# Kernel optimization log

Hardware: AMD Instinct MI355X
Metric: run time of the kernel (lower is better)

## Reference

```python
import jax, jax.numpy as jnp
import numpy as np

B, L, D, H, S = 4, 4096, 1024, 16, 4
DH = D // H


def setup_inputs() -> dict:
    key = jax.random.key(0)
    ks = jax.random.split(key, 12)
    std = 0.02
    inp = {
        "x": jax.random.normal(ks[0], (B, L, D), jnp.float32),
        "scale_logits": jax.random.normal(ks[1], (S,), jnp.float32),
        "wq": jax.random.normal(ks[2], (D, D), jnp.float32) * std,
        "bq": jnp.zeros((D,), jnp.float32),
        "wk": jax.random.normal(ks[3], (D, D), jnp.float32) * std,
        "bk": jnp.zeros((D,), jnp.float32),
        "wv": jax.random.normal(ks[4], (D, D), jnp.float32) * std,
        "bv": jnp.zeros((D,), jnp.float32),
        "wo": jax.random.normal(ks[5], (D, D), jnp.float32) * std,
        "bo": jnp.zeros((D,), jnp.float32),
        "ws": jax.random.normal(ks[6], (S, D, D), jnp.float32) * std,  # per-scale Linear weights (out,in)
        "bs": jax.random.normal(ks[7], (S, D), jnp.float32) * std,
    }
    return inp


def reference(x, scale_logits, wq, bq, wk, bk, wv, bv, wo, bo, ws, bs):
    # q/k/v projections; kept flat (B,L,D) since the torch code re-flattens before scale proj
    qf = x @ wq.T + bq
    kf = x @ wk.T + bk
    vf = x @ wv.T + bv
    # per-scale linear projection, vectorized over scales: (B,S,L,D)
    sq = jnp.einsum('bld,sed->bsle', qf, ws) + bs[None, :, None, :]
    sk = jnp.einsum('bld,sed->bsle', kf, ws) + bs[None, :, None, :]
    sv = jnp.einsum('bld,sed->bsle', vf, ws) + bs[None, :, None, :]
    sq = sq.reshape(B, S, L, H, DH)
    sk = sk.reshape(B, S, L, H, DH)
    sv = sv.reshape(B, S, L, H, DH)
    # faithful to torch: matmul over last two dims of (B,L,H,dh) -> per-position
    # head-mixing scores of shape (B,S,L,H,H)
    scale = 1.0 / np.sqrt(DH).astype(np.float32)
    scores = jnp.einsum('bslhd,bslgd->bslhg', sq, sk) * scale
    attn = jax.nn.softmax(scores, axis=-1)
    out = jnp.einsum('bslhg,bslgd->bslhd', attn, sv)  # (B,S,L,H,DH)
    w = jax.nn.softmax(scale_logits, axis=0)  # (S,)
    combined = jnp.einsum('s,bslhd->blhd', w, out).reshape(B, L, D)
    return combined @ wo.T + bo
```

## Files before the change

### kernel.cpp

```cpp
#include <hip/hip_runtime.h>


typedef unsigned short u16;
typedef __attribute__((ext_vector_type(8))) short s16x8;
typedef __attribute__((ext_vector_type(8))) unsigned short u16x8;
typedef __attribute__((ext_vector_type(4))) float f32x4;

#define MM 16384
#define DDIM 1024
#define DDSQ 1048576ull

__device__ __forceinline__ u16 f2bf(float f) {
  unsigned u = __float_as_uint(f);
  u = (u + 0x7FFFu + ((u >> 16) & 1u)) >> 16;
  return (u16)u;
}
__device__ __forceinline__ float b2f(u16 b) {
  return __uint_as_float(((unsigned)b) << 16);
}
__device__ __forceinline__ void gload_lds16(const void* g, void* l) {
  __builtin_amdgcn_global_load_lds(
      (const __attribute__((address_space(1))) void*)g,
      (__attribute__((address_space(3))) void*)l, 16, 0, 0);
}

__global__ __launch_bounds__(256) void k_f32_to_bf16(
    const float* __restrict__ in, u16* __restrict__ out, int n4) {
  int i = blockIdx.x * 256 + threadIdx.x;
  if (i >= n4) return;
  float4 v = reinterpret_cast<const float4*>(in)[i];
  ushort4 o;
  o.x = f2bf(v.x); o.y = f2bf(v.y); o.z = f2bf(v.z); o.w = f2bf(v.w);
  reinterpret_cast<ushort4*>(out)[i] = o;
}

__global__ __launch_bounds__(256) void k_transpose_bf16(
    const float* __restrict__ wq, const float* __restrict__ wk,
    const float* __restrict__ wv, u16* __restrict__ out) {
  __shared__ float tile[32][33];
  const float* src = (blockIdx.z == 0) ? wq : (blockIdx.z == 1) ? wk : wv;
  u16* dst = out + (size_t)blockIdx.z * DDSQ;
  int tx = threadIdx.x, ty = threadIdx.y;
  int bx = blockIdx.x * 32, by = blockIdx.y * 32;
#pragma unroll
  for (int i = 0; i < 4; ++i)
    tile[ty + 8 * i][tx] = src[(size_t)(by + ty + 8 * i) * DDIM + bx + tx];
  __syncthreads();
#pragma unroll
  for (int i = 0; i < 4; ++i)
    dst[(size_t)(bx + ty + 8 * i) * DDIM + by + tx] = f2bf(tile[tx][ty + 8 * i]);
}

__global__ __launch_bounds__(256) void k_bias_fuse(
    const float* __restrict__ ws, const float* __restrict__ bq,
    const float* __restrict__ bk, const float* __restrict__ bv,
    const float* __restrict__ bs, float* __restrict__ bf) {
  int idx = blockIdx.y;
  int s = idx / 3, t = idx - s * 3;
  const float* bt = (t == 0) ? bq : (t == 1) ? bk : bv;
  int lane = threadIdx.x & 63, wid = threadIdx.x >> 6;
  int e = blockIdx.x * 4 + wid;
  const float* wr = ws + (size_t)s * DDSQ + (size_t)e * DDIM;
  float p = 0.f;
  for (int j = lane; j < DDIM; j += 64) p += wr[j] * bt[j];
#pragma unroll
  for (int off = 32; off > 0; off >>= 1) p += __shfl_xor(p, off);
  if (lane == 0) bf[idx * DDIM + e] = p + bs[s * DDIM + e];
}

template <typename OutT>
__global__ __launch_bounds__(256) void k_gemm_bt(
    const u16* __restrict__ A, const u16* __restrict__ B, OutT* __restrict__ C,
    const float* __restrict__ bias, int M, int N, int K,
    size_t za, size_t zb, size_t zc, size_t zbias, int zmode) {
  __shared__ u16 lds_a[128 * 32];
  __shared__ u16 lds_b[128 * 32];

  int z = blockIdx.x >> 3;
  int n_blk = blockIdx.x & 7;
  int m_blk = blockIdx.y;
  if (zmode == 1) { A += (size_t)(z / 3) * za; B += (size_t)(z % 3) * zb; }
  else            { A += (size_t)z * za;       B += (size_t)z * zb; }
  C += (size_t)z * zc;
  const float* biasz = bias ? (bias + (size_t)z * zbias) : nullptr;

  int m0 = m_blk * 128, n0 = n_blk * 128;
  int tid = threadIdx.x;
  int lane = tid & 63, wid = tid >> 6;
  int wm = wid >> 1, wn = wid & 1;

  f32x4 acc[4][4] = {};

  auto stage = [&](int k0) {
#pragma unroll
    for (int i = 0; i < 2; ++i) {
      int c = wid * 2 + i;
      int row = c * 16 + (lane >> 2);
      int col = (lane & 3) * 8;
      gload_lds16(A + (size_t)(m0 + row) * K + k0 + col, &lds_a[c * 512]);
      gload_lds16(B + (size_t)(n0 + row) * K + k0 + col, &lds_b[c * 512]);
    }
  };

  stage(0);
  int ar = (wm * 64 + (lane & 15)) * 32 + (lane >> 4) * 8;
  int br = (wn * 64 + (lane & 15)) * 32 + (lane >> 4) * 8;
  for (int k0 = 0;;) {
    __syncthreads();
    s16x8 af[4], bfr[4];
#pragma unroll
    for (int mi = 0; mi < 4; ++mi)
      af[mi] = *reinterpret_cast<const s16x8*>(&lds_a[ar + mi * 16 * 32]);
#pragma unroll
    for (int ni = 0; ni < 4; ++ni)
      bfr[ni] = *reinterpret_cast<const s16x8*>(&lds_b[br + ni * 16 * 32]);
#pragma unroll
    for (int mi = 0; mi < 4; ++mi)
#pragma unroll
      for (int ni = 0; ni < 4; ++ni)
        acc[mi][ni] = __builtin_amdgcn_mfma_f32_16x16x32_bf16(
            af[mi], bfr[ni], acc[mi][ni], 0, 0, 0);
    k0 += 32;
    if (k0 >= K) break;
    __syncthreads();
    stage(k0);
  }

#pragma unroll
  for (int mi = 0; mi < 4; ++mi) {
#pragma unroll
    for (int ni = 0; ni < 4; ++ni) {
      int colg = n0 + wn * 64 + ni * 16 + (lane & 15);
      float badd = biasz ? biasz[colg] : 0.f;
#pragma unroll
      for (int r = 0; r < 4; ++r) {
        int rowg = m0 + wm * 64 + mi * 16 + ((lane >> 4) << 2) + r;
        float v = acc[mi][ni][r] + badd;
        if constexpr (sizeof(OutT) == 2) C[(size_t)rowg * N + colg] = f2bf(v);
        else                             C[(size_t)rowg * N + colg] = v;
      }
    }
  }
}

__global__ __launch_bounds__(512, 2) void k_gemm256(
    const u16* __restrict__ A, const u16* __restrict__ B, u16* __restrict__ C,
    const float* __restrict__ bias, int M, int N, int K,
    size_t za, size_t zb, size_t zc, size_t zbias, int nbx) {
  __shared__ u16 lds[3][2][8192];

  int z = blockIdx.x / nbx;
  int nb = blockIdx.x - z * nbx;
  const u16* Ag = A + (size_t)z * za;
  const u16* Bg = B + (size_t)z * zb;
  u16* Cg = C + (size_t)z * zc;
  const float* biasz = bias + (size_t)z * zbias;

  int m0 = blockIdx.y * 256, n0 = nb * 256;
  int tid = threadIdx.x;
  int lane = tid & 63, wid = tid >> 6;
  int wm = wid >> 2, wn = wid & 3;
  int NT = K >> 5;

  int scb = ((lane & 3) * 16) ^ (((lane >> 3) & 3) << 4);
  const char* srcA[2]; const char* srcB[2]; int ldsc[2];
#pragma unroll
  for (int r = 0; r < 2; ++r) {
    int c = r * 8 + wid;
    int row = c * 16 + (lane >> 2);
    srcA[r] = (const char*)Ag + ((size_t)(m0 + row) * K) * 2 + scb;
    srcB[r] = (const char*)Bg + ((size_t)(n0 + row) * K) * 2 + scb;
    ldsc[r] = c * 1024;
  }
  char* lbase = (char*)&lds[0][0][0];

  int fxor = ((lane >> 4) * 16) ^ (((lane >> 1) & 3) << 4);
  int aoff = (wm * 128 + (lane & 15)) * 64 + fxor;
  int boff = (wn * 64 + (lane & 15)) * 64 + fxor;

  f32x4 acc[8][4] = {};

#define STAGE_A(kt, rg)                                                   \
  {                                                                       \
    _Pragma("unroll") for (int r = 0; r < 2; ++r)                         \
        gload_lds16(srcA[r] + (size_t)(kt) * 64,                          \
                    lbase + (rg) * 32768 + ldsc[r]);                      \
  }
#define STAGE_B(kt, rg)                                                   \
  {                                                                       \
    _Pragma("unroll") for (int r = 0; r < 2; ++r)                         \
        gload_lds16(srcB[r] + (size_t)(kt) * 64,                          \
                    lbase + (rg) * 32768 + 16384 + ldsc[r]);              \
  }

  STAGE_A(0, 0); STAGE_B(0, 0);
  STAGE_A(1, 1); STAGE_B(1, 1);
  __builtin_amdgcn_sched_barrier(0);
  asm volatile("s_waitcnt vmcnt(4)" ::: "memory");
  __builtin_amdgcn_sched_barrier(0);
  __builtin_amdgcn_s_barrier();

  int ring = 0;
  for (int t = 0; t < NT; ++t) {
    int t2 = (t + 2 < NT) ? t + 2 : NT - 1;
    int rg2 = ring + 2; if (rg2 >= 3) rg2 -= 3;
    const char* bA = lbase + ring * 32768;
    const char* bB = bA + 16384;

    s16x8 fb[4], fa[4];
#pragma unroll
    for (int ni = 0; ni < 4; ++ni)
      fb[ni] = *(const s16x8*)(bB + boff + ni * 1024);
#pragma unroll
    for (int mi = 0; mi < 4; ++mi)
      fa[mi] = *(const s16x8*)(bA + aoff + mi * 1024);
    STAGE_A(t2, rg2);
    __builtin_amdgcn_sched_barrier(0);
    __builtin_amdgcn_s_barrier();
    asm volatile("s_waitcnt lgkmcnt(0)" ::: "memory");
    __builtin_amdgcn_sched_barrier(0);
    __builtin_amdgcn_s_setprio(1);
#pragma unroll
    for (int mi = 0; mi < 4; ++mi)
#pragma unroll
      for (int ni = 0; ni < 4; ++ni)
        acc[mi][ni] = __builtin_amdgcn_mfma_f32_16x16x32_bf16(
            fa[mi], fb[ni], acc[mi][ni], 0, 0, 0);
    __builtin_amdgcn_s_setprio(0);
    __builtin_amdgcn_sched_barrier(0);
    __builtin_amdgcn_s_barrier();

    s16x8 fa2[4];
#pragma unroll
    for (int mi = 0; mi < 4; ++mi)
      fa2[mi] = *(const s16x8*)(bA + aoff + 4096 + mi * 1024);
    STAGE_B(t2, rg2);
    __builtin_amdgcn_sched_barrier(0);
    asm volatile("s_waitcnt vmcnt(4)" ::: "memory");
    __builtin_amdgcn_sched_barrier(0);
    __builtin_amdgcn_s_barrier();
    asm volatile("s_waitcnt lgkmcnt(0)" ::: "memory");
    __builtin_amdgcn_sched_barrier(0);
    __builtin_amdgcn_s_setprio(1);
#pragma unroll
    for (int mi = 0; mi < 4; ++mi)
#pragma unroll
      for (int ni = 0; ni < 4; ++ni)
        acc[mi + 4][ni] = __builtin_amdgcn_mfma_f32_16x16x32_bf16(
            fa2[mi], fb[ni], acc[mi + 4][ni], 0, 0, 0);
    __builtin_amdgcn_s_setprio(0);
    __builtin_amdgcn_sched_barrier(0);
    __builtin_amdgcn_s_barrier();

    ring = ring + 1; if (ring == 3) ring = 0;
  }
#undef STAGE_A
#undef STAGE_B

#pragma unroll
  for (int mi = 0; mi < 8; ++mi) {
#pragma unroll
    for (int ni = 0; ni < 4; ++ni) {
      int colg = n0 + wn * 64 + ni * 16 + (lane & 15);
      float badd = biasz[colg];
#pragma unroll
      for (int r = 0; r < 4; ++r) {
        int rowg = m0 + wm * 128 + mi * 16 + ((lane >> 4) << 2) + r;
        Cg[(size_t)rowg * N + colg] = f2bf(acc[mi][ni][r] + badd);
      }
    }
  }
}

__global__ __launch_bounds__(256) void k_attn_all(
    const u16* __restrict__ proj, u16* __restrict__ outbf,
    const float* __restrict__ sl, int rows) {
  __shared__ u16 kv[4][2][1024];
  int lane = threadIdx.x & 63, wid = threadIdx.x >> 6;
  int row = blockIdx.x * 4 + wid;
  int h = lane >> 2, dq = lane & 3;
  int doff = h * 64 + dq * 16;

  float l0 = sl[0], l1 = sl[1], l2 = sl[2], l3 = sl[3];
  float lm = fmaxf(fmaxf(l0, l1), fmaxf(l2, l3));
  float e0 = __expf(l0 - lm), e1 = __expf(l1 - lm), e2 = __expf(l2 - lm),
        e3 = __expf(l3 - lm);
  float esum = e0 + e1 + e2 + e3;
  float wsc4[4] = {e0 / esum, e1 / esum, e2 / esum, e3 / esum};

  float acc[16];
#pragma unroll
  for (int i = 0; i < 16; ++i) acc[i] = 0.f;

  for (int s = 0; s < 4; ++s) {
    const u16* kr = proj + ((size_t)(3 * s + 1) * rows + row) * DDIM;
    const u16* vr = proj + ((size_t)(3 * s + 2) * rows + row) * DDIM;
    asm volatile("s_waitcnt vmcnt(0) lgkmcnt(0)" ::: "memory");
    gload_lds16(kr + lane * 8,       &kv[wid][0][0]);
    gload_lds16(kr + 512 + lane * 8, &kv[wid][0][512]);
    gload_lds16(vr + lane * 8,       &kv[wid][1][0]);
    gload_lds16(vr + 512 + lane * 8, &kv[wid][1][512]);

    const u16* qr = proj + ((size_t)(3 * s) * rows + row) * DDIM + doff;
    u16x8 q0 = *reinterpret_cast<const u16x8*>(qr);
    u16x8 q1 = *reinterpret_cast<const u16x8*>(qr + 8);
    float qf[16];
#pragma unroll
    for (int i = 0; i < 8; ++i) {
      qf[i]     = b2f(q0[i]) * 0.125f;
      qf[8 + i] = b2f(q1[i]) * 0.125f;
    }
    asm volatile("s_waitcnt vmcnt(0)" ::: "memory");

    float sc[16];
#pragma unroll
    for (int g = 0; g < 16; ++g) {
      const u16* kp = &kv[wid][0][g * 64 + dq * 16];
      u16x8 k0 = *reinterpret_cast<const u16x8*>(kp);
      u16x8 k1 = *reinterpret_cast<const u16x8*>(kp + 8);
      float d = 0.f;
#pragma unroll
      for (int i = 0; i < 8; ++i) d = fmaf(qf[i], b2f(k0[i]), d);
#pragma unroll
      for (int i = 0; i < 8; ++i) d = fmaf(qf[8 + i], b2f(k1[i]), d);
      d += __shfl_xor(d, 1);
      d += __shfl_xor(d, 2);
      sc[g] = d;
    }

    float mx = sc[0];
#pragma unroll
    for (int g = 1; g < 16; ++g) mx = fmaxf(mx, sc[g]);
    float sum = 0.f;
#pragma unroll
    for (int g = 0; g < 16; ++g) { sc[g] = __expf(sc[g] - mx); sum += sc[g]; }
    float inv = wsc4[s] / sum;
#pragma unroll
    for (int g = 0; g < 16; ++g) sc[g] *= inv;

#pragma unroll
    for (int g = 0; g < 16; ++g) {
      float a = sc[g];
      const u16* vp = &kv[wid][1][g * 64 + dq * 16];
      u16x8 v0 = *reinterpret_cast<const u16x8*>(vp);
      u16x8 v1 = *reinterpret_cast<const u16x8*>(vp + 8);
#pragma unroll
      for (int i = 0; i < 8; ++i) {
        acc[i]     = fmaf(a, b2f(v0[i]), acc[i]);
        acc[8 + i] = fmaf(a, b2f(v1[i]), acc[8 + i]);
      }
    }
  }

  u16* op = outbf + (size_t)row * DDIM + doff;
  u16x8 o0, o1;
#pragma unroll
  for (int i = 0; i < 8; ++i) {
    o0[i] = f2bf(acc[i]);
    o1[i] = f2bf(acc[8 + i]);
  }
  *reinterpret_cast<u16x8*>(op) = o0;
  *reinterpret_cast<u16x8*>(op + 8) = o1;
}

extern "C" void kernel_launch(void* const* d_in, const int* in_sizes, int n_in,
                              void* d_out, int out_size, void* d_ws,
                              size_t ws_size, hipStream_t stream) {
  const float* x  = (const float*)d_in[0];
  const float* sl = (const float*)d_in[1];
  const float* wq = (const float*)d_in[2];
  const float* bq = (const float*)d_in[3];
  const float* wk = (const float*)d_in[4];
  const float* bk = (const float*)d_in[5];
  const float* wv = (const float*)d_in[6];
  const float* bv = (const float*)d_in[7];
  const float* wo = (const float*)d_in[8];
  const float* bo = (const float*)d_in[9];
  const float* ws = (const float*)d_in[10];
  const float* bs = (const float*)d_in[11];
  float* out = (float*)d_out;

  char* wsb = (char*)d_ws;
  size_t off = 0;
  u16* xbf    = (u16*)(wsb + off); off += (size_t)MM * DDIM * 2;
  u16* wfus   = (u16*)(wsb + off); off += 12ull * DDSQ * 2;
  u16* wobf   = (u16*)(wsb + off); off += DDSQ * 2;
  float* bfus = (float*)(wsb + off); off += 65536;
  u16* combc  = (u16*)(wsb + off); off += (size_t)MM * DDIM * 2;
  char* dynr  = wsb + off;
  size_t fixed = off;

  int chunk = 4096;
  while (chunk > 1024 && fixed + (size_t)12 * chunk * DDIM * 2 > ws_size)
    chunk >>= 1;
  u16* projc = (u16*)dynr;
  u16* wtT  = (u16*)dynr;
  u16* wsbf = (u16*)(dynr + 3ull * DDSQ * 2);

  int n4;
  n4 = MM * DDIM / 4;
  k_f32_to_bf16<<<(n4 + 255) / 256, 256, 0, stream>>>(x, xbf, n4);
  n4 = (int)(4 * DDSQ / 4);
  k_f32_to_bf16<<<(n4 + 255) / 256, 256, 0, stream>>>(ws, wsbf, n4);
  n4 = (int)(DDSQ / 4);
  k_f32_to_bf16<<<(n4 + 255) / 256, 256, 0, stream>>>(wo, wobf, n4);

  k_transpose_bf16<<<dim3(32, 32, 3), dim3(32, 8), 0, stream>>>(wq, wk, wv, wtT);
  k_bias_fuse<<<dim3(256, 12), 256, 0, stream>>>(ws, bq, bk, bv, bs, bfus);

  k_gemm_bt<u16><<<dim3(96, 8), 256, 0, stream>>>(
      wsbf, wtT, wfus, nullptr, 1024, 1024, 1024, DDSQ, DDSQ, DDSQ, 0, 1);

  int nchunks = MM / chunk;
  for (int c = 0; c < nchunks; ++c) {
    const u16* xa = xbf + (size_t)c * chunk * DDIM;
    k_gemm256<<<dim3(48, chunk / 256), 512, 0, stream>>>(
        xa, wfus, projc, bfus, chunk, 1024, 1024,
        0, DDSQ, (size_t)chunk * DDIM, DDIM, 4);
    k_attn_all<<<dim3(chunk / 4), 256, 0, stream>>>(
        projc, combc + (size_t)c * chunk * DDIM, sl, chunk);
  }

  k_gemm_bt<float><<<dim3(8, 128), 256, 0, stream>>>(
      combc, wobf, out, bo, MM, 1024, 1024, 0, 0, 0, 0, 0);
}
```

Measured before the change: 754.4 us.

## Deepen GEMM LDS ring to four stages and reuse it for output projection

The 256x256 bf16 GEMM now uses a four-slot LDS ring with three tiles prefetched ahead. Each k-step has one vmcnt wait plus one barrier instead of several barriers split around two MFMA halves. The kernel is templated on output type so the final fp32 output projection runs through this large-tile kernel instead of the generic k_gemm_bt. The extra LDS stage forces occupancy down to one block per CU and leans on compiler-inserted LDS waits, which may limit latency hiding.

```diff
diff --git a/kernel.cpp b/kernel.cpp
--- a/kernel.cpp
+++ b/kernel.cpp
@@ -143,17 +143,18 @@
   }
 }
 
-__global__ __launch_bounds__(512, 2) void k_gemm256(
-    const u16* __restrict__ A, const u16* __restrict__ B, u16* __restrict__ C,
+template <typename OutT>
+__global__ __launch_bounds__(512, 1) void k_gemm256(
+    const u16* __restrict__ A, const u16* __restrict__ B, OutT* __restrict__ C,
     const float* __restrict__ bias, int M, int N, int K,
     size_t za, size_t zb, size_t zc, size_t zbias, int nbx) {
-  __shared__ u16 lds[3][2][8192];
+  __shared__ u16 lds[4][2][8192];
 
   int z = blockIdx.x / nbx;
   int nb = blockIdx.x - z * nbx;
   const u16* Ag = A + (size_t)z * za;
   const u16* Bg = B + (size_t)z * zb;
-  u16* Cg = C + (size_t)z * zc;
+  OutT* Cg = C + (size_t)z * zc;
   const float* biasz = bias + (size_t)z * zbias;
 
   int m0 = blockIdx.y * 256, n0 = nb * 256;
@@ -195,30 +196,30 @@
 
   STAGE_A(0, 0); STAGE_B(0, 0);
   STAGE_A(1, 1); STAGE_B(1, 1);
-  __builtin_amdgcn_sched_barrier(0);
-  asm volatile("s_waitcnt vmcnt(4)" ::: "memory");
-  __builtin_amdgcn_sched_barrier(0);
-  __builtin_amdgcn_s_barrier();
-
-  int ring = 0;
+  STAGE_A(2, 2); STAGE_B(2, 2);
+  asm volatile("s_waitcnt vmcnt(8)" ::: "memory");
+  asm volatile("s_barrier" ::: "memory");
+
   for (int t = 0; t < NT; ++t) {
-    int t2 = (t + 2 < NT) ? t + 2 : NT - 1;
-    int rg2 = ring + 2; if (rg2 >= 3) rg2 -= 3;
-    const char* bA = lbase + ring * 32768;
+    int rg = t & 3;
+    int t3 = (t + 3 < NT) ? t + 3 : NT - 1;
+    int rg3 = (rg + 3) & 3;
+    const char* bA = lbase + rg * 32768;
     const char* bB = bA + 16384;
 
-    s16x8 fb[4], fa[4];
+    s16x8 fb[4], fa[4], fa2[4];
 #pragma unroll
     for (int ni = 0; ni < 4; ++ni)
       fb[ni] = *(const s16x8*)(bB + boff + ni * 1024);
 #pragma unroll
     for (int mi = 0; mi < 4; ++mi)
       fa[mi] = *(const s16x8*)(bA + aoff + mi * 1024);
-    STAGE_A(t2, rg2);
-    __builtin_amdgcn_sched_barrier(0);
-    __builtin_amdgcn_s_barrier();
-    asm volatile("s_waitcnt lgkmcnt(0)" ::: "memory");
-    __builtin_amdgcn_sched_barrier(0);
+    STAGE_A(t3, rg3);
+#pragma unroll
+    for (int mi = 0; mi < 4; ++mi)
+      fa2[mi] = *(const s16x8*)(bA + aoff + 4096 + mi * 1024);
+    STAGE_B(t3, rg3);
+
     __builtin_amdgcn_s_setprio(1);
 #pragma unroll
     for (int mi = 0; mi < 4; ++mi)
@@ -226,22 +227,6 @@
       for (int ni = 0; ni < 4; ++ni)
         acc[mi][ni] = __builtin_amdgcn_mfma_f32_16x16x32_bf16(
             fa[mi], fb[ni], acc[mi][ni], 0, 0, 0);
-    __builtin_amdgcn_s_setprio(0);
-    __builtin_amdgcn_sched_barrier(0);
-    __builtin_amdgcn_s_barrier();
-
-    s16x8 fa2[4];
-#pragma unroll
-    for (int mi = 0; mi < 4; ++mi)
-      fa2[mi] = *(const s16x8*)(bA + aoff + 4096 + mi * 1024);
-    STAGE_B(t2, rg2);
-    __builtin_amdgcn_sched_barrier(0);
-    asm volatile("s_waitcnt vmcnt(4)" ::: "memory");
-    __builtin_amdgcn_sched_barrier(0);
-    __builtin_amdgcn_s_barrier();
-    asm volatile("s_waitcnt lgkmcnt(0)" ::: "memory");
-    __builtin_amdgcn_sched_barrier(0);
-    __builtin_amdgcn_s_setprio(1);
 #pragma unroll
     for (int mi = 0; mi < 4; ++mi)
 #pragma unroll
@@ -249,13 +234,14 @@
         acc[mi + 4][ni] = __builtin_amdgcn_mfma_f32_16x16x32_bf16(
             fa2[mi], fb[ni], acc[mi + 4][ni], 0, 0, 0);
     __builtin_amdgcn_s_setprio(0);
-    __builtin_amdgcn_sched_barrier(0);
-    __builtin_amdgcn_s_barrier();
-
-    ring = ring + 1; if (ring == 3) ring = 0;
+
+    asm volatile("s_waitcnt vmcnt(8)" ::: "memory");
+    asm volatile("s_barrier" ::: "memory");
   }
 #undef STAGE_A
 #undef STAGE_B
+
+  asm volatile("s_waitcnt vmcnt(0)" ::: "memory");
 
 #pragma unroll
   for (int mi = 0; mi < 8; ++mi) {
@@ -266,7 +252,9 @@
 #pragma unroll
       for (int r = 0; r < 4; ++r) {
         int rowg = m0 + wm * 128 + mi * 16 + ((lane >> 4) << 2) + r;
-        Cg[(size_t)rowg * N + colg] = f2bf(acc[mi][ni][r] + badd);
+        float v = acc[mi][ni][r] + badd;
+        if constexpr (sizeof(OutT) == 2) Cg[(size_t)rowg * N + colg] = f2bf(v);
+        else                             Cg[(size_t)rowg * N + colg] = v;
       }
     }
   }
@@ -414,13 +402,13 @@
   int nchunks = MM / chunk;
   for (int c = 0; c < nchunks; ++c) {
     const u16* xa = xbf + (size_t)c * chunk * DDIM;
-    k_gemm256<<<dim3(48, chunk / 256), 512, 0, stream>>>(
+    k_gemm256<u16><<<dim3(48, chunk / 256), 512, 0, stream>>>(
         xa, wfus, projc, bfus, chunk, 1024, 1024,
         0, DDSQ, (size_t)chunk * DDIM, DDIM, 4);
     k_attn_all<<<dim3(chunk / 4), 256, 0, stream>>>(
         projc, combc + (size_t)c * chunk * DDIM, sl, chunk);
   }
 
-  k_gemm_bt<float><<<dim3(8, 128), 256, 0, stream>>>(
-      combc, wobf, out, bo, MM, 1024, 1024, 0, 0, 0, 0, 0);
-}
+  k_gemm256<float><<<dim3(4, 64), 512, 0, stream>>>(
+      combc, wobf, out, bo, MM, 1024, 1024, 0, 0, 0, 0, 4);
+}
```

Result: faster. 723.4 us (-4.1%).
